# Performance work log

Measured on AMD Instinct MI355X. Metric: run time of the kernel, lower is better.

## Reference

```python
import jax, jax.numpy as jnp
import numpy as np

N_NODES = 50000
N_EDGES = 800000
D_IN = 128
HEADS = 8
UNITS = 16


def setup_inputs() -> dict:
    key = jax.random.key(0)
    ks = jax.random.split(key, 6)
    x = jax.random.normal(ks[0], (N_NODES, D_IN), dtype=jnp.float32)
    edges = jax.random.randint(ks[1], (N_EDGES, 2), 0, N_NODES, dtype=jnp.int32)
    # glorot_uniform-style init for kernels
    lim_k = float(np.sqrt(6.0 / (D_IN + HEADS * UNITS)))
    kernel = jax.random.uniform(ks[2], (D_IN, HEADS, UNITS), minval=-lim_k, maxval=lim_k, dtype=jnp.float32)
    lim_a = float(np.sqrt(6.0 / (1 + HEADS * UNITS)))
    kernel_attention1 = jax.random.uniform(ks[3], (1, HEADS, UNITS), minval=-lim_a, maxval=lim_a, dtype=jnp.float32)
    bias_attention = jnp.zeros((1, HEADS, UNITS), dtype=jnp.float32)
    bias = jnp.zeros((HEADS * UNITS,), dtype=jnp.float32)
    return {"x": x, "edges": edges, "kernel": kernel,
            "kernel_attention1": kernel_attention1,
            "bias_attention": bias_attention, "bias": bias}


def reference(x, edges, kernel, kernel_attention1, bias_attention, bias):
    # GATv2 (version=2), merge_type='concat', use_bias=True, training=False
    n_nodes = x.shape[0]
    sources = edges[:, 0]
    targets = edges[:, 1]

    xp = jnp.einsum('nd,dhu->nhu', x, kernel)          # [N, H, U]
    xbias = xp + bias_attention                        # [N, H, U]

    # per-edge attention score: leaky_relu(x_t + x_s) . a   (GATv2)
    s = jax.nn.leaky_relu(xbias[targets] + xbias[sources], negative_slope=0.2)  # [E, H, U]
    scores = jnp.sum(s * kernel_attention1, axis=-1)   # [E, H]

    # segment softmax over incoming edges of each target node
    smax = jax.ops.segment_max(scores, targets, num_segments=n_nodes)  # [N, H]
    scores = jnp.exp(scores - smax[targets])
    ssum = jax.ops.segment_sum(scores, targets, num_segments=n_nodes)  # [N, H]
    scores = scores / (ssum[targets] + 1e-7)           # [E, H]

    # weighted scatter-aggregate of source features
    out = jax.ops.segment_sum(scores[..., None] * xp[sources], targets,
                              num_segments=n_nodes)    # [N, H, U]
    out = out.reshape(n_nodes, HEADS * UNITS) + bias   # concat heads
    return jax.nn.gelu(out, approximate=True)
```

## Files before the change

### kernel.cpp

```cpp
#include <hip/hip_runtime.h>
#include <hip/hip_fp16.h>


#define CAP   64
#define CAPB  48
#define SB    242
#define NBK   196

typedef float f32x4 __attribute__((ext_vector_type(4)));
typedef int   i32x4 __attribute__((ext_vector_type(4)));

__device__ __forceinline__ uint2 pack_half4(float4 v) {
    __half2 a = __floats2half2_rn(v.x, v.y);
    __half2 b = __floats2half2_rn(v.z, v.w);
    uint2 r;
    r.x = *(unsigned int*)&a;
    r.y = *(unsigned int*)&b;
    return r;
}

__device__ __forceinline__ float4 unpack_half4(uint2 r) {
    __half2 a = *(__half2*)&r.x;
    __half2 b = *(__half2*)&r.y;
    const float2 fa = __half22float2(a);
    const float2 fb = __half22float2(b);
    return make_float4(fa.x, fa.y, fb.x, fb.y);
}

__device__ __forceinline__ float gelu_tanh(float x) {
    const float y = 0.7978845608028654f * fmaf(0.044715f * x, x * x, x);
    const float e = __expf(2.f * y);
    const float th = 1.f - 2.f / (e + 1.f);
    return 0.5f * x * (1.f + th);
}


__global__ __launch_bounds__(256) void gemm_bucket(
    const float* __restrict__ x, const float* __restrict__ w,
    const int* __restrict__ edges,
    unsigned short* __restrict__ xph,
    unsigned int* __restrict__ bkt, int* __restrict__ bbc,
    int N, int E) {
    __shared__ unsigned int smem[NBK * CAPB + NBK];
    const int tid = threadIdx.x;
    const int bid = blockIdx.x;

    if (bid >= SB) {
        float* xl = (float*)smem;
        const int rb = (bid - SB) << 6;
        const f32x4* x4 = (const f32x4*)x;
        for (int i = tid; i < 64 * 32; i += 256) {
            const int r = i >> 5, c = i & 31;
            const int row = rb + r;
            f32x4 v = (f32x4)(0.f);
            if (row < N) v = __builtin_nontemporal_load(&x4[(size_t)row * 32 + c]);
            float* dst = &xl[r * 129 + c * 4];
            dst[0] = v.x; dst[1] = v.y; dst[2] = v.z; dst[3] = v.w;
        }
        __syncthreads();

        const int lane = tid & 63;
        const int wv = __builtin_amdgcn_readfirstlane(tid >> 6);
        const int cb = wv << 5;
        const int r8 = lane >> 3;
        const int c8 = lane & 7;

        f32x4 acc[8];
#pragma unroll
        for (int i = 0; i < 8; ++i) acc[i] = (f32x4)(0.f);

        const float* xbase = &xl[r8 * 129];
        const float* wbase = w + cb + (c8 << 2);

#pragma unroll 4
        for (int k = 0; k < 128; ++k) {
            const f32x4 wv4 = *(const f32x4*)(wbase + (k << 7));
#pragma unroll
            for (int i = 0; i < 8; ++i) {
                const float xv = xbase[i * (8 * 129) + k];
                acc[i] += xv * wv4;
            }
        }

        unsigned short* op = xph + cb + (c8 << 2);
#pragma unroll
        for (int i = 0; i < 8; ++i) {
            const int row = rb + r8 + (i << 3);
            if (row < N) {
                *(uint2*)(op + (size_t)row * 128) =
                    pack_half4(make_float4(acc[i].x, acc[i].y,
                                           acc[i].z, acc[i].w));
            }
        }
    } else {
        const int sb = bid;
        unsigned int* eb = smem;
        int* hist = (int*)(smem + NBK * CAPB);
        const int pairs = E >> 1;
        const int chunk = (pairs + SB - 1) / SB;
        const int p0 = sb * chunk;
        const int p1 = min(pairs, p0 + chunk);
        const i32x4* __restrict__ e4 = (const i32x4*)edges;

        if (tid < NBK) hist[tid] = 0;
        __syncthreads();
        for (int i = p0 + tid; i < p1; i += 256) {
            const i32x4 v = __builtin_nontemporal_load(&e4[i]);
            const int b0 = v.y >> 8;
            const int q0 = atomicAdd(&hist[b0], 1);
            if (q0 < CAPB)
                eb[b0 * CAPB + q0] =
                    ((unsigned int)v.x << 8) | (unsigned int)(v.y & 255);
            const int b1 = v.w >> 8;
            const int q1 = atomicAdd(&hist[b1], 1);
            if (q1 < CAPB)
                eb[b1 * CAPB + q1] =
                    ((unsigned int)v.z << 8) | (unsigned int)(v.w & 255);
        }
        __syncthreads();
        const int wv = tid >> 6, lane = tid & 63;
        for (int lb = wv; lb < NBK; lb += 4) {
            const int ce = min(hist[lb], CAPB);
            if (lane < ce)
                bkt[((size_t)lb * SB + sb) * CAPB + lane] = eb[lb * CAPB + lane];
        }
        if (tid < NBK) bbc[tid * SB + sb] = min(hist[tid], CAPB);
    }
}


__global__ __launch_bounds__(512) void build_lists(
    const unsigned int* __restrict__ bkt, const int* __restrict__ bbc,
    int* __restrict__ cnt, unsigned short* __restrict__ srcs, int N) {
    __shared__ int lst[256 * CAP];
    __shared__ int cl[256];
    __shared__ int cA[SB];
    const int b = blockIdx.x;
    const int tid = threadIdx.x;

    if (tid < 256) cl[tid] = 0;
    if (tid < SB) cA[tid] = bbc[b * SB + tid];
    __syncthreads();

    const int wv = tid >> 6, lane = tid & 63;
    for (int kk = 0; kk < 32; kk += 4) {
        int ce[4];
        unsigned int ev[4];
#pragma unroll
        for (int u = 0; u < 4; ++u) {
            const int sb = wv + ((kk + u) << 3);
            ce[u] = (sb < SB) ? cA[sb] : 0;
            ev[u] = (lane < ce[u])
                        ? bkt[((size_t)b * SB + sb) * CAPB + lane]
                        : 0u;
        }
#pragma unroll
        for (int u = 0; u < 4; ++u) {
            if (lane < ce[u]) {
                const int ni = ev[u] & 255;
                const int pos = atomicAdd(&cl[ni], 1);
                lst[(ni << 6) + pos] = (int)(ev[u] >> 8);
            }
        }
    }
    __syncthreads();

    const int nb = b << 8;
    if (tid < 256 && nb + tid < N) cnt[nb + tid] = cl[tid];
    for (int i = tid; i < 256 * CAP; i += 512) {
        if (nb + (i >> 6) < N)
            srcs[((size_t)nb << 6) + i] = (unsigned short)lst[i];
    }
}


__device__ __forceinline__ void edge_accum4(const float4 xs, const float4 base,
                                            const float4 k6, const float4 k4,
                                            const float mask,
                                            float4& acc, float& ssum) {
    const float a0 = base.x + xs.x;
    const float a1 = base.y + xs.y;
    const float a2 = base.z + xs.z;
    const float a3 = base.w + xs.w;
    float p = a0 * k6.x;
    p = fmaf(fabsf(a0), k4.x, p);
    p = fmaf(a1, k6.y, p);
    p = fmaf(fabsf(a1), k4.y, p);
    p = fmaf(a2, k6.z, p);
    p = fmaf(fabsf(a2), k4.z, p);
    p = fmaf(a3, k6.w, p);
    p = fmaf(fabsf(a3), k4.w, p);
    p += __shfl_xor(p, 1);
    p += __shfl_xor(p, 2);
    const float esc = exp2f(p) * mask;
    acc.x = fmaf(esc, xs.x, acc.x);
    acc.y = fmaf(esc, xs.y, acc.y);
    acc.z = fmaf(esc, xs.z, acc.z);
    acc.w = fmaf(esc, xs.w, acc.w);
    ssum += esc;
}

__global__ __launch_bounds__(256) void gather_pad(
    const unsigned short* __restrict__ xph, const int* __restrict__ cnt,
    const unsigned short* __restrict__ srcs, const float* __restrict__ katt,
    const float* __restrict__ batt, const float* __restrict__ bias,
    float* __restrict__ out, int N) {
    const int node = (blockIdx.x * blockDim.x + threadIdx.x) >> 6;
    const int lane = threadIdx.x & 63;
    if (node >= N) return;
    const int c = lane & 31;
    const int half = lane >> 5;

    const int len = cnt[node];
    const int sv = srcs[((size_t)node << 6) + lane];

    const uint2* __restrict__ xp4 = (const uint2*)xph;
    const float4 xt = unpack_half4(xp4[(size_t)node * 32 + c]);
    const float4 ka = ((const float4*)katt)[c];
    const float4 ba = ((const float4*)batt)[c];
    const float L2E = 1.4426950408889634f;
    float4 k6, k4;
    k6.x = 0.6f * L2E * ka.x; k4.x = 0.4f * L2E * ka.x;
    k6.y = 0.6f * L2E * ka.y; k4.y = 0.4f * L2E * ka.y;
    k6.z = 0.6f * L2E * ka.z; k4.z = 0.4f * L2E * ka.z;
    k6.w = 0.6f * L2E * ka.w; k4.w = 0.4f * L2E * ka.w;
    float4 base;
    base.x = xt.x + 2.f * ba.x;
    base.y = xt.y + 2.f * ba.y;
    base.z = xt.z + 2.f * ba.z;
    base.w = xt.w + 2.f * ba.w;

    float4 acc = make_float4(0.f, 0.f, 0.f, 0.f);
    float ssum = 0.f;

    int jj = 0;
    for (; jj + 8 <= len; jj += 8) {
        const int s0 = __shfl(sv, jj + half);
        const int s1 = __shfl(sv, jj + 2 + half);
        const int s2 = __shfl(sv, jj + 4 + half);
        const int s3 = __shfl(sv, jj + 6 + half);
        const uint2 r0 = xp4[(size_t)s0 * 32 + c];
        const uint2 r1 = xp4[(size_t)s1 * 32 + c];
        const uint2 r2 = xp4[(size_t)s2 * 32 + c];
        const uint2 r3 = xp4[(size_t)s3 * 32 + c];
        edge_accum4(unpack_half4(r0), base, k6, k4, 1.f, acc, ssum);
        edge_accum4(unpack_half4(r1), base, k6, k4, 1.f, acc, ssum);
        edge_accum4(unpack_half4(r2), base, k6, k4, 1.f, acc, ssum);
        edge_accum4(unpack_half4(r3), base, k6, k4, 1.f, acc, ssum);
    }
    for (; jj + 4 <= len; jj += 4) {
        const int s0 = __shfl(sv, jj + half);
        const int s1 = __shfl(sv, jj + 2 + half);
        const uint2 r0 = xp4[(size_t)s0 * 32 + c];
        const uint2 r1 = xp4[(size_t)s1 * 32 + c];
        edge_accum4(unpack_half4(r0), base, k6, k4, 1.f, acc, ssum);
        edge_accum4(unpack_half4(r1), base, k6, k4, 1.f, acc, ssum);
    }
    for (; jj < len; jj += 2) {
        const int j = jj + half;
        int s = __shfl(sv, j & 63);
        const bool valid = (j < len);
        s = valid ? s : 0;
        const uint2 rr = xp4[(size_t)s * 32 + c];
        edge_accum4(unpack_half4(rr), base, k6, k4, valid ? 1.f : 0.f, acc, ssum);
    }

    acc.x += __shfl_xor(acc.x, 32);
    acc.y += __shfl_xor(acc.y, 32);
    acc.z += __shfl_xor(acc.z, 32);
    acc.w += __shfl_xor(acc.w, 32);
    ssum  += __shfl_xor(ssum, 32);

    if (half == 0) {
        const float inv = 1.f / (ssum + 1e-7f);
        const float4 b = ((const float4*)bias)[c];
        f32x4 o;
        o.x = gelu_tanh(fmaf(acc.x, inv, b.x));
        o.y = gelu_tanh(fmaf(acc.y, inv, b.y));
        o.z = gelu_tanh(fmaf(acc.z, inv, b.z));
        o.w = gelu_tanh(fmaf(acc.w, inv, b.w));
        __builtin_nontemporal_store(o, &((f32x4*)out)[(size_t)node * 32 + c]);
    }
}


extern "C" void kernel_launch(void* const* d_in, const int* in_sizes, int n_in,
                              void* d_out, int out_size, void* d_ws, size_t ws_size,
                              hipStream_t stream) {
    const float* x    = (const float*)d_in[0];
    const int*   edg  = (const int*)d_in[1];
    const float* kern = (const float*)d_in[2];
    const float* katt = (const float*)d_in[3];
    const float* batt = (const float*)d_in[4];
    const float* bias = (const float*)d_in[5];

    const int N = in_sizes[0] / 128;
    const int E = in_sizes[1] / 2;

    float* out = (float*)d_out;
    unsigned short* xph = (unsigned short*)d_ws;
    int* cnt = (int*)(xph + (size_t)N * 128);
    unsigned short* srcs16 = (unsigned short*)(cnt + N);
    int* bbc = (int*)(srcs16 + (size_t)N * CAP);
    unsigned int* bkt = (unsigned int*)(bbc + (size_t)NBK * SB);

    const int gemmB = (N + 63) / 64;
    gemm_bucket<<<SB + gemmB, 256, 0, stream>>>(x, kern, edg, xph, bkt, bbc,
                                                N, E);
    build_lists<<<NBK, 512, 0, stream>>>(bkt, bbc, cnt, srcs16, N);
    gather_pad<<<(N * 64 + 255) / 256, 256, 0, stream>>>(xph, cnt, srcs16,
                                                         katt, batt, bias,
                                                         out, N);
}
```

Measured before the change: 160.3 us.

## Compute node projection GEMM with fp16 MFMA instead of scalar FMA

Replaces the fp32 outer-product GEMM for x@W with MFMA 16x16x32 f16 instructions. Each wave loads its 16 rows of x straight into registers as fp16 A fragments. W is converted to fp16 and rearranged in shared memory into B-fragment layout. The goal is to cut the ALU-bound FMA loop in the GEMM blocks, at the cost of rounding x and W to fp16 before multiplying and of scattered 2-byte output stores.

```diff
diff --git a/kernel.cpp b/kernel.cpp
--- a/kernel.cpp
+++ b/kernel.cpp
@@ -7,8 +7,9 @@
 #define SB    242
 #define NBK   196
 
-typedef float f32x4 __attribute__((ext_vector_type(4)));
-typedef int   i32x4 __attribute__((ext_vector_type(4)));
+typedef float    f32x4 __attribute__((ext_vector_type(4)));
+typedef int      i32x4 __attribute__((ext_vector_type(4)));
+typedef _Float16 f16x8 __attribute__((ext_vector_type(8)));
 
 __device__ __forceinline__ uint2 pack_half4(float4 v) {
     __half2 a = __floats2half2_rn(v.x, v.y);
@@ -46,50 +47,65 @@
     const int bid = blockIdx.x;
 
     if (bid >= SB) {
-        float* xl = (float*)smem;
         const int rb = (bid - SB) << 6;
-        const f32x4* x4 = (const f32x4*)x;
-        for (int i = tid; i < 64 * 32; i += 256) {
-            const int r = i >> 5, c = i & 31;
-            const int row = rb + r;
-            f32x4 v = (f32x4)(0.f);
-            if (row < N) v = __builtin_nontemporal_load(&x4[(size_t)row * 32 + c]);
-            float* dst = &xl[r * 129 + c * 4];
-            dst[0] = v.x; dst[1] = v.y; dst[2] = v.z; dst[3] = v.w;
+        const int lane = tid & 63;
+        const int wv   = tid >> 6;
+        const int m    = lane & 15;
+        const int oct  = lane >> 4;
+
+        int row = rb + (wv << 4) + m;
+        row = min(row, N - 1);
+        const float* xg = x + (size_t)row * 128 + (oct << 3);
+        f16x8 a[4];
+#pragma unroll
+        for (int t = 0; t < 4; ++t) {
+            const f32x4 u0 = *(const f32x4*)(xg + t * 32);
+            const f32x4 u1 = *(const f32x4*)(xg + t * 32 + 4);
+            f16x8 av;
+            av[0] = (_Float16)u0.x; av[1] = (_Float16)u0.y;
+            av[2] = (_Float16)u0.z; av[3] = (_Float16)u0.w;
+            av[4] = (_Float16)u1.x; av[5] = (_Float16)u1.y;
+            av[6] = (_Float16)u1.z; av[7] = (_Float16)u1.w;
+            a[t] = av;
+        }
+
+        _Float16* wl = (_Float16*)smem;
+        const f32x4* w4 = (const f32x4*)w;
+        for (int i = tid; i < 4096; i += 256) {
+            const f32x4 v = w4[i];
+            const int k = i >> 5, c0 = (i & 31) << 2;
+            const int t = k >> 5, ko = (k >> 3) & 3, j = k & 7;
+            const int n16 = c0 >> 4, lb = (ko << 4) + (c0 & 15);
+            _Float16* dst = wl + (((t << 3) + n16) << 9) + (lb << 3) + j;
+            dst[0]  = (_Float16)v.x;
+            dst[8]  = (_Float16)v.y;
+            dst[16] = (_Float16)v.z;
+            dst[24] = (_Float16)v.w;
         }
         __syncthreads();
 
-        const int lane = tid & 63;
-        const int wv = __builtin_amdgcn_readfirstlane(tid >> 6);
-        const int cb = wv << 5;
-        const int r8 = lane >> 3;
-        const int c8 = lane & 7;
-
         f32x4 acc[8];
 #pragma unroll
-        for (int i = 0; i < 8; ++i) acc[i] = (f32x4)(0.f);
-
-        const float* xbase = &xl[r8 * 129];
-        const float* wbase = w + cb + (c8 << 2);
-
-#pragma unroll 4
-        for (int k = 0; k < 128; ++k) {
-            const f32x4 wv4 = *(const f32x4*)(wbase + (k << 7));
-#pragma unroll
-            for (int i = 0; i < 8; ++i) {
-                const float xv = xbase[i * (8 * 129) + k];
-                acc[i] += xv * wv4;
+        for (int n16 = 0; n16 < 8; ++n16) {
+            f32x4 c = (f32x4)(0.f);
+#pragma unroll
+            for (int t = 0; t < 4; ++t) {
+                const f16x8 b = *(const f16x8*)(
+                    wl + (((t << 3) + n16) << 9) + (lane << 3));
+                c = __builtin_amdgcn_mfma_f32_16x16x32_f16(a[t], b, c, 0, 0, 0);
             }
-        }
-
-        unsigned short* op = xph + cb + (c8 << 2);
-#pragma unroll
-        for (int i = 0; i < 8; ++i) {
-            const int row = rb + r8 + (i << 3);
-            if (row < N) {
-                *(uint2*)(op + (size_t)row * 128) =
-                    pack_half4(make_float4(acc[i].x, acc[i].y,
-                                           acc[i].z, acc[i].w));
+            acc[n16] = c;
+        }
+
+        const int orow0 = rb + (wv << 4) + (oct << 2);
+#pragma unroll
+        for (int n16 = 0; n16 < 8; ++n16) {
+#pragma unroll
+            for (int i = 0; i < 4; ++i) {
+                const int r = orow0 + i;
+                if (r < N)
+                    xph[(size_t)r * 128 + (n16 << 4) + m] =
+                        __half_as_ushort(__float2half(acc[n16][i]));
             }
         }
     } else {
```

New measurement: 148.3 us. 7.5% less time.
